# Optimization experiments

Hardware: AMD Instinct MI355X
Metric: run time of the kernel (lower is better)

Reference implementation:

```python
import jax, jax.numpy as jnp
import numpy as np

NNODES = 128
BS = 1024
MAX_ST = (NNODES + 1) ** 2   # 16641
MAX_ST1 = NNODES ** 2        # 16384
AT_LEN = NNODES + 1          # 129
MAXOUT = AT_LEN + MAX_ST + MAX_ST1  # 33154
HIDDEN = 512
OUT_DIM = AT_LEN             # 129


def setup_inputs() -> dict:
    key = jax.random.key(0)
    ks = jax.random.split(key, 6)
    st = jax.random.normal(ks[0], (BS, MAX_ST), dtype=jnp.float32)
    at = jax.random.normal(ks[1], (BS, AT_LEN), dtype=jnp.float32)
    st1 = jax.random.normal(ks[2], (BS, MAX_ST1), dtype=jnp.float32)
    # MLP params (self.layers): Linear(MAXOUT->HIDDEN) + ReLU + Linear(HIDDEN->OUT_DIM)
    W1 = jax.random.normal(ks[3], (MAXOUT, HIDDEN), dtype=jnp.float32) * (1.0 / np.sqrt(MAXOUT))
    b1 = jnp.zeros((HIDDEN,), dtype=jnp.float32)
    W2 = jax.random.normal(ks[4], (HIDDEN, OUT_DIM), dtype=jnp.float32) * (1.0 / np.sqrt(HIDDEN))
    b2 = jnp.zeros((OUT_DIM,), dtype=jnp.float32)
    return {"st": st, "at": at, "st1": st1, "W1": W1, "b1": b1, "W2": W2, "b2": b2}


def reference(st, at, st1, W1, b1, W2, b2):
    # Batched equivalent of the per-sample Python loop:
    # per sample: cat(pad(st.flatten(), maxSt), at, pad(st1.flatten(), maxSt1)) -> layers -> cat outputs.
    # st/st1 are already at padded sizes here, so concat directly along features.
    x = jnp.concatenate([st, at, st1], axis=1)          # [B, MAXOUT]
    h = jax.nn.relu(x @ W1 + b1)                        # [B, HIDDEN]
    out = h @ W2 + b2                                   # [B, OUT_DIM]
    return out.reshape(-1)                              # concatenated 1-D outputs, matching torch.cat
```

## Files before the change

kernel.cpp:

```cpp
#include <hip/hip_runtime.h>

#define BATCH 1024
#define STSZ 16641
#define ATSZ 129
#define ST1SZ 16384
#define K1 33154
#define K1P 33280
#define HID 512
#define ODIM 129
#define NKT 520
#define NSLICE 16

typedef __bf16 bf16;
typedef bf16 bf16x8 __attribute__((ext_vector_type(8)));
typedef float floatx4 __attribute__((ext_vector_type(4)));
typedef float f32x4u __attribute__((ext_vector_type(4), aligned(4)));

typedef __attribute__((address_space(3))) unsigned int as3_uint;
typedef __attribute__((address_space(1))) unsigned int as1_uint;

__device__ __forceinline__ unsigned short f2bf(float f) {
  unsigned int u = __float_as_uint(f);
  unsigned int r = (u + 0x7FFFu + ((u >> 16) & 1u)) >> 16;
  return (unsigned short)r;
}

__device__ __forceinline__ void gload_lds16(const unsigned short* g, unsigned short* l) {
  __builtin_amdgcn_global_load_lds((const as1_uint*)g, (as3_uint*)l, 16, 0, 0);
}

__global__ __launch_bounds__(256) void packX(const float* __restrict__ st,
                                             const float* __restrict__ at,
                                             const float* __restrict__ st1,
                                             unsigned short* __restrict__ Xb) {
  int b = blockIdx.y;
  int g = blockIdx.x * 256 + threadIdx.x;
  if (g >= K1P / 4) return;
  int col = g * 4;
  const float* srow  = st  + (long)b * STSZ;
  const float* arow  = at  + (long)b * ATSZ;
  const float* s1row = st1 + (long)b * ST1SZ;

  float4 v;
  if (col + 3 < STSZ) {
    f32x4u t = *(const f32x4u*)(srow + col);
    v = make_float4(t.x, t.y, t.z, t.w);
  } else if (col >= STSZ + ATSZ && col + 3 < K1) {
    f32x4u t = *(const f32x4u*)(s1row + (col - (STSZ + ATSZ)));
    v = make_float4(t.x, t.y, t.z, t.w);
  } else if (col >= STSZ && col + 3 < STSZ + ATSZ) {
    f32x4u t = *(const f32x4u*)(arow + (col - STSZ));
    v = make_float4(t.x, t.y, t.z, t.w);
  } else if (col >= K1) {
    v = make_float4(0.f, 0.f, 0.f, 0.f);
  } else {
    float e[4];
#pragma unroll
    for (int j = 0; j < 4; ++j) {
      int p = col + j;
      if (p < STSZ)                 e[j] = srow[p];
      else if (p < STSZ + ATSZ)     e[j] = arow[p - STSZ];
      else if (p < K1)              e[j] = s1row[p - (STSZ + ATSZ)];
      else                          e[j] = 0.f;
    }
    v = make_float4(e[0], e[1], e[2], e[3]);
  }
  unsigned short o[4] = { f2bf(v.x), f2bf(v.y), f2bf(v.z), f2bf(v.w) };
  *(ushort4*)&Xb[(long)b * K1P + col] = *(const ushort4*)o;
}

__global__ __launch_bounds__(256) void packW1(const float* __restrict__ W1,
                                              unsigned short* __restrict__ W1t) {
  __shared__ unsigned short tile[64][72];
  int k0 = blockIdx.x * 64;
  int n0 = blockIdx.y * 64;
  int tid = threadIdx.x;
  int nt = (tid & 15) * 4;
  int kr = tid >> 4;
#pragma unroll
  for (int p = 0; p < 4; ++p) {
    int k = p * 16 + kr;
    int kk = k0 + k;
    float4 v = make_float4(0.f, 0.f, 0.f, 0.f);
    if (kk < K1) v = *(const float4*)&W1[(long)kk * HID + n0 + nt];
    unsigned short o[4] = { f2bf(v.x), f2bf(v.y), f2bf(v.z), f2bf(v.w) };
    *(ushort4*)&tile[k][nt] = *(const ushort4*)o;
  }
  __syncthreads();
  int kt = (tid & 15) * 4;
  int nr = tid >> 4;
#pragma unroll
  for (int p = 0; p < 4; ++p) {
    int n = p * 16 + nr;
    unsigned short o[4] = { tile[kt][n], tile[kt + 1][n], tile[kt + 2][n], tile[kt + 3][n] };
    *(ushort4*)&W1t[(long)(n0 + n) * K1P + k0 + kt] = *(const ushort4*)o;
  }
}

__global__ __launch_bounds__(256, 2) void gemm1(const unsigned short* __restrict__ Xb,
                                                const unsigned short* __restrict__ W1t,
                                                float* __restrict__ part) {
  __shared__ __align__(16) unsigned short lA[128 * 64];
  __shared__ __align__(16) unsigned short lB[128 * 64];

  int nt = blockIdx.x;
  int mt = blockIdx.y;
  int s  = blockIdx.z;
  int t0 = s * 32 + (s < 8 ? s : 8);
  int tc = 32 + (s < 8 ? 1 : 0);

  int tid = threadIdx.x;
  int wave = tid >> 6;
  int lane = tid & 63;
  int wm = (wave & 1) * 64;
  int wn = (wave >> 1) * 64;

  floatx4 acc[4][4] = {};

  const unsigned short* Ab = Xb  + (long)(mt * 128) * K1P;
  const unsigned short* Bb = W1t + (long)(nt * 128) * K1P;

  int srow = (lane >> 3);
  int scol = (lane & 7) * 8;

  for (int it = 0; it < tc; ++it) {
    long kOff = (long)(t0 + it) * 64;
#pragma unroll
    for (int r = 0; r < 4; ++r) {
      int c = wave * 4 + r;
      int row = c * 8 + srow;
      gload_lds16(Ab + (long)row * K1P + kOff + scol, &lA[c * 512 + lane * 8]);
      gload_lds16(Bb + (long)row * K1P + kOff + scol, &lB[c * 512 + lane * 8]);
    }
    __syncthreads();
#pragma unroll
    for (int ks = 0; ks < 2; ++ks) {
      int kcol = ks * 32 + (lane >> 4) * 8;
      bf16x8 af[4], bfr[4];
#pragma unroll
      for (int i = 0; i < 4; ++i)
        af[i] = *(const bf16x8*)&lA[(wm + i * 16 + (lane & 15)) * 64 + kcol];
#pragma unroll
      for (int j = 0; j < 4; ++j)
        bfr[j] = *(const bf16x8*)&lB[(wn + j * 16 + (lane & 15)) * 64 + kcol];
#pragma unroll
      for (int i = 0; i < 4; ++i)
#pragma unroll
        for (int j = 0; j < 4; ++j)
          acc[i][j] = __builtin_amdgcn_mfma_f32_16x16x32_bf16(af[i], bfr[j], acc[i][j], 0, 0, 0);
    }
    __syncthreads();
  }

  float* P = part + (long)s * BATCH * HID;
  int cn = nt * 128 + wn + (lane & 15);
  int rbase = mt * 128 + wm + (lane >> 4) * 4;
#pragma unroll
  for (int i = 0; i < 4; ++i)
#pragma unroll
    for (int j = 0; j < 4; ++j)
#pragma unroll
      for (int r = 0; r < 4; ++r)
        P[(long)(rbase + i * 16 + r) * HID + cn + j * 16] = acc[i][j][r];
}

__global__ __launch_bounds__(256) void reduceBias(const float* __restrict__ part,
                                                  const float* __restrict__ b1,
                                                  float* __restrict__ h) {
  int e = blockIdx.x * 256 + threadIdx.x;
  float a = b1[e & (HID - 1)];
#pragma unroll
  for (int s = 0; s < NSLICE; ++s) a += part[(long)s * BATCH * HID + e];
  h[e] = fmaxf(a, 0.0f);
}

__global__ __launch_bounds__(256) void gemm2(const float* __restrict__ h,
                                             const float* __restrict__ W2,
                                             const float* __restrict__ b2,
                                             float* __restrict__ out) {
  __shared__ float hs[HID];
  int m = blockIdx.x;
  int t = threadIdx.x;
#pragma unroll
  for (int i = t; i < HID; i += 256) hs[i] = h[(long)m * HID + i];
  __syncthreads();
  if (t < ODIM) {
    float a = b2[t];
#pragma unroll 8
    for (int k = 0; k < HID; ++k) a += hs[k] * W2[k * ODIM + t];
    out[(long)m * ODIM + t] = a;
  }
}

extern "C" void kernel_launch(void* const* d_in, const int* in_sizes, int n_in,
                              void* d_out, int out_size, void* d_ws, size_t ws_size,
                              hipStream_t stream) {
  const float* st  = (const float*)d_in[0];
  const float* at  = (const float*)d_in[1];
  const float* st1 = (const float*)d_in[2];
  const float* W1  = (const float*)d_in[3];
  const float* b1  = (const float*)d_in[4];
  const float* W2  = (const float*)d_in[5];
  const float* b2  = (const float*)d_in[6];
  float* out = (float*)d_out;

  char* ws = (char*)d_ws;
  unsigned short* Xb  = (unsigned short*)ws;
  unsigned short* W1t = (unsigned short*)(ws + (size_t)BATCH * K1P * 2);
  float* part = (float*)(ws + (size_t)BATCH * K1P * 2 + (size_t)HID * K1P * 2);
  float* h    = part + (size_t)NSLICE * BATCH * HID;

  packX<<<dim3((K1P / 4 + 255) / 256, BATCH), 256, 0, stream>>>(st, at, st1, Xb);
  packW1<<<dim3(NKT, HID / 64), 256, 0, stream>>>(W1, W1t);
  gemm1<<<dim3(4, 8, NSLICE), 256, 0, stream>>>(Xb, W1t, part);
  reduceBias<<<dim3(BATCH * HID / 256), 256, 0, stream>>>(part, b1, h);
  gemm2<<<dim3(BATCH), 256, 0, stream>>>(h, W2, b2, out);
}
```

Measured before the change: 329.3 us.

## Swizzle LDS layout, double split-K slices, store bf16 partials, vectorize reduction

Applies an XOR swizzle to the LDS tile column index in gemm1 to cut bank conflicts on the bf16x8 fragment reads. Split-K goes from 16 to 32 slices, which gives 1024 blocks instead of 512 on the GPU, and partial sums are stored as bf16 to halve the partial-buffer traffic. The reduction kernel now reads 4 elements per thread. Rounding each partial to bf16 adds numerical error in exchange for the lower bandwidth.

```diff
diff --git a/kernel.cpp b/kernel.cpp
--- a/kernel.cpp
+++ b/kernel.cpp
@@ -9,7 +9,7 @@
 #define HID 512
 #define ODIM 129
 #define NKT 520
-#define NSLICE 16
+#define NSLICE 32
 
 typedef __bf16 bf16;
 typedef bf16 bf16x8 __attribute__((ext_vector_type(8)));
@@ -23,6 +23,10 @@
   unsigned int u = __float_as_uint(f);
   unsigned int r = (u + 0x7FFFu + ((u >> 16) & 1u)) >> 16;
   return (unsigned short)r;
+}
+__device__ __forceinline__ float bf2f(unsigned short s) {
+  unsigned int u = ((unsigned int)s) << 16;
+  return __uint_as_float(u);
 }
 
 __device__ __forceinline__ void gload_lds16(const unsigned short* g, unsigned short* l) {
@@ -99,15 +103,15 @@
 
 __global__ __launch_bounds__(256, 2) void gemm1(const unsigned short* __restrict__ Xb,
                                                 const unsigned short* __restrict__ W1t,
-                                                float* __restrict__ part) {
+                                                unsigned short* __restrict__ part) {
   __shared__ __align__(16) unsigned short lA[128 * 64];
   __shared__ __align__(16) unsigned short lB[128 * 64];
 
   int nt = blockIdx.x;
   int mt = blockIdx.y;
   int s  = blockIdx.z;
-  int t0 = s * 32 + (s < 8 ? s : 8);
-  int tc = 32 + (s < 8 ? 1 : 0);
+  int t0 = s * 16 + (s < 8 ? s : 8);
+  int tc = 16 + (s < 8 ? 1 : 0);
 
   int tid = threadIdx.x;
   int wave = tid >> 6;
@@ -120,8 +124,10 @@
   const unsigned short* Ab = Xb  + (long)(mt * 128) * K1P;
   const unsigned short* Bb = W1t + (long)(nt * 128) * K1P;
 
-  int srow = (lane >> 3);
-  int scol = (lane & 7) * 8;
+  int srow = lane >> 3;
+  int scol = ((lane & 7) ^ srow) * 8;
+
+  int sr = lane & 7;
 
   for (int it = 0; it < tc; ++it) {
     long kOff = (long)(t0 + it) * 64;
@@ -135,14 +141,15 @@
     __syncthreads();
 #pragma unroll
     for (int ks = 0; ks < 2; ++ks) {
-      int kcol = ks * 32 + (lane >> 4) * 8;
+      int q = ks * 4 + (lane >> 4);
+      int kidx = ((q ^ sr)) * 8;
       bf16x8 af[4], bfr[4];
 #pragma unroll
       for (int i = 0; i < 4; ++i)
-        af[i] = *(const bf16x8*)&lA[(wm + i * 16 + (lane & 15)) * 64 + kcol];
+        af[i] = *(const bf16x8*)&lA[(wm + i * 16 + (lane & 15)) * 64 + kidx];
 #pragma unroll
       for (int j = 0; j < 4; ++j)
-        bfr[j] = *(const bf16x8*)&lB[(wn + j * 16 + (lane & 15)) * 64 + kcol];
+        bfr[j] = *(const bf16x8*)&lB[(wn + j * 16 + (lane & 15)) * 64 + kidx];
 #pragma unroll
       for (int i = 0; i < 4; ++i)
 #pragma unroll
@@ -152,7 +159,7 @@
     __syncthreads();
   }
 
-  float* P = part + (long)s * BATCH * HID;
+  unsigned short* P = part + (long)s * BATCH * HID;
   int cn = nt * 128 + wn + (lane & 15);
   int rbase = mt * 128 + wm + (lane >> 4) * 4;
 #pragma unroll
@@ -161,17 +168,22 @@
     for (int j = 0; j < 4; ++j)
 #pragma unroll
       for (int r = 0; r < 4; ++r)
-        P[(long)(rbase + i * 16 + r) * HID + cn + j * 16] = acc[i][j][r];
-}
-
-__global__ __launch_bounds__(256) void reduceBias(const float* __restrict__ part,
+        P[(long)(rbase + i * 16 + r) * HID + cn + j * 16] = f2bf(acc[i][j][r]);
+}
+
+__global__ __launch_bounds__(256) void reduceBias(const unsigned short* __restrict__ part,
                                                   const float* __restrict__ b1,
                                                   float* __restrict__ h) {
-  int e = blockIdx.x * 256 + threadIdx.x;
-  float a = b1[e & (HID - 1)];
-#pragma unroll
-  for (int s = 0; s < NSLICE; ++s) a += part[(long)s * BATCH * HID + e];
-  h[e] = fmaxf(a, 0.0f);
+  int e4 = blockIdx.x * 256 + threadIdx.x;
+  float4 a = ((const float4*)b1)[e4 & (HID / 4 - 1)];
+#pragma unroll
+  for (int s = 0; s < NSLICE; ++s) {
+    ushort4 p = ((const ushort4*)part)[(long)s * (BATCH * HID / 4) + e4];
+    a.x += bf2f(p.x); a.y += bf2f(p.y); a.z += bf2f(p.z); a.w += bf2f(p.w);
+  }
+  a.x = fmaxf(a.x, 0.f); a.y = fmaxf(a.y, 0.f);
+  a.z = fmaxf(a.z, 0.f); a.w = fmaxf(a.w, 0.f);
+  ((float4*)h)[e4] = a;
 }
 
 __global__ __launch_bounds__(256) void gemm2(const float* __restrict__ h,
@@ -205,14 +217,15 @@
   float* out = (float*)d_out;
 
   char* ws = (char*)d_ws;
-  unsigned short* Xb  = (unsigned short*)ws;
-  unsigned short* W1t = (unsigned short*)(ws + (size_t)BATCH * K1P * 2);
-  float* part = (float*)(ws + (size_t)BATCH * K1P * 2 + (size_t)HID * K1P * 2);
-  float* h    = part + (size_t)NSLICE * BATCH * HID;
+  unsigned short* Xb   = (unsigned short*)ws;
+  unsigned short* W1t  = (unsigned short*)(ws + (size_t)BATCH * K1P * 2);
+  unsigned short* part = (unsigned short*)(ws + (size_t)BATCH * K1P * 2 + (size_t)HID * K1P * 2);
+  float* h = (float*)(ws + (size_t)BATCH * K1P * 2 + (size_t)HID * K1P * 2
+                      + (size_t)NSLICE * BATCH * HID * 2);
 
   packX<<<dim3((K1P / 4 + 255) / 256, BATCH), 256, 0, stream>>>(st, at, st1, Xb);
   packW1<<<dim3(NKT, HID / 64), 256, 0, stream>>>(W1, W1t);
   gemm1<<<dim3(4, 8, NSLICE), 256, 0, stream>>>(Xb, W1t, part);
-  reduceBias<<<dim3(BATCH * HID / 256), 256, 0, stream>>>(part, b1, h);
+  reduceBias<<<dim3(BATCH * HID / 4 / 256), 256, 0, stream>>>(part, b1, h);
   gemm2<<<dim3(BATCH), 256, 0, stream>>>(h, W2, b2, out);
 }
```

Result: no change. 326.8 us (-0.8%).
